# Kernel tuning notes

Hardware: AMD Instinct MI355X
Metric: run time of the kernel (lower is better)

Reference implementation:

```python
import jax, jax.numpy as jnp
import numpy as np
from jax import lax

KERNEL = 21
SHIFT = KERNEL - 1  # 20
NUM_LEVELS = 2
EPS = 1e-5
NEG_SLOPE = 0.01


def _conv1d(x, w):
    # x: [B, Cin, T], w: [Cout, Cin, K] -> [B, Cout, T-K+1]
    return lax.conv_general_dilated(x, w, window_strides=(1,), padding='VALID',
                                    dimension_numbers=('NCH', 'OIH', 'NCH'))


def _batchnorm_train(x, gamma, beta):
    # training-mode BN over (N, L) per channel, biased variance (torch semantics)
    mean = jnp.mean(x, axis=(0, 2), keepdims=True)
    var = jnp.mean((x - mean) ** 2, axis=(0, 2), keepdims=True)
    return (x - mean) * lax.rsqrt(var + EPS) * gamma[None, :, None] + beta[None, :, None]


def _spp(y, L, num_levels, pool):
    # y: [B, C, Tc]; L: [B] valid lengths. Level i has 2^i bins:
    #   bin j covers [j*floor(L/2^i), j*floor(L/2^i)+ceil(L/2^i)), matching
    #   F.max_pool1d/avg_pool1d(kernel=ceil(f), stride=floor(f)) on x[:, :, :L].
    B, C, Tc = y.shape
    pos = jnp.arange(Tc)[None, :]                     # [1, Tc]
    Lf = L.astype(jnp.float32)
    outs = []
    for i in range(num_levels):
        k = 2 ** i
        f = Lf / k
        stride = jnp.floor(f).astype(jnp.int32)        # [B]
        kern = jnp.ceil(f).astype(jnp.int32)           # [B]
        bins = []
        for j in range(k):
            start = j * stride                         # [B]
            mask = (pos >= start[:, None]) & (pos < (start + kern)[:, None])  # [B, Tc]
            m = mask[:, None, :]                       # [B, 1, Tc]
            if pool == 'max':
                bins.append(jnp.max(jnp.where(m, y, -jnp.inf), axis=-1))      # [B, C]
            else:
                s = jnp.sum(jnp.where(m, y, jnp.zeros((), y.dtype)), axis=-1)
                bins.append(s / kern[:, None].astype(y.dtype))
        # torch .view flattens (C, k) channel-major
        outs.append(jnp.stack(bins, axis=-1).reshape(B, C * k))
    return jnp.concatenate(outs, axis=1)               # [B, C*(2^n - 1)]


def setup_inputs() -> dict:
    key = jax.random.key(0)
    k1, k2, k3, k4, k5 = jax.random.split(key, 5)
    B, C, T = 32, 64, 16384
    n_tasks = 2
    n_lin = 2 * C * (2 ** NUM_LEVELS - 1)  # 384
    x = jax.random.normal(k1, (B, C, T), dtype=jnp.float32)
    orig_len = jax.random.randint(k2, (B,), T // 2, T + 1, dtype=jnp.int32)
    w1 = jax.random.normal(k3, (C, C, KERNEL), dtype=jnp.float32) * 0.05
    w2 = jax.random.normal(k4, (C, C, KERNEL), dtype=jnp.float32) * 0.05
    g1 = jnp.ones((C,), jnp.float32); b1 = jnp.zeros((C,), jnp.float32)
    g2 = jnp.ones((C,), jnp.float32); b2 = jnp.zeros((C,), jnp.float32)
    fc_w = jax.random.normal(k5, (n_tasks, n_lin), dtype=jnp.float32) * 0.05
    fc_b = jnp.zeros((n_tasks,), jnp.float32)
    return {"x": x, "orig_len": orig_len, "w1": w1, "g1": g1, "b1": b1,
            "w2": w2, "g2": g2, "b2": b2, "fc_w": fc_w, "fc_b": fc_b}


def reference(x, orig_len, w1, g1, b1, w2, g2, b2, fc_w, fc_b):
    L = orig_len - SHIFT  # valid conv-output length per sample
    y1 = jax.nn.leaky_relu(_batchnorm_train(_conv1d(x, w1), g1, b1), NEG_SLOPE)
    p1 = _spp(y1, L, NUM_LEVELS, 'max')
    y2 = jax.nn.leaky_relu(_batchnorm_train(_conv1d(x, w2), g2, b2), NEG_SLOPE)
    p2 = _spp(y2, L, NUM_LEVELS, 'avg')
    feat = jnp.concatenate([p1, p2], axis=1)           # [B, 384]
    return feat @ fc_w.T + fc_b
```

## Files before the change

kernel.cpp:

```cpp
#include <hip/hip_runtime.h>

#define AS1 __attribute__((address_space(1)))
#define AS3 __attribute__((address_space(3)))

using u16 = unsigned short;
using u32 = unsigned int;
typedef __attribute__((ext_vector_type(8))) short bf16x8;
typedef __attribute__((ext_vector_type(4))) float f32x4;

constexpr int Bn    = 32;
constexpr int Tn    = 16384;
constexpr int TCn   = 16364;
constexpr int TILE  = 256;
constexpr int XROWS = 280;
constexpr int TPAD  = 16416;

__device__ __forceinline__ u16 f2bf(float f) {
  union { float f; u32 u; } v; v.f = f;
  u32 u = v.u;
  u += 0x7fffu + ((u >> 16) & 1u);
  return (u16)(u >> 16);
}
__device__ __forceinline__ float bf2f(u32 h) {
  union { u32 u; float f; } v; v.u = h << 16; return v.f;
}
__device__ __forceinline__ u32 encf(float f) {
  union { float f; u32 u; } v; v.f = f;
  return (v.u & 0x80000000u) ? ~v.u : (v.u | 0x80000000u);
}
__device__ __forceinline__ float decf(u32 u) {
  union { u32 u; float f; } v;
  v.u = (u & 0x80000000u) ? (u ^ 0x80000000u) : ~u;
  return v.f;
}
__device__ __forceinline__ void gload_lds16(const void* g, void* l) {
  __builtin_amdgcn_global_load_lds((const AS1 u32*)g, (AS3 u32*)l, 16, 0, 0);
}
__device__ __forceinline__ float leaky(float z) { return z > 0.f ? z : 0.01f * z; }

__global__ __launch_bounds__(256) void transpose_x(const float* __restrict__ x,
                                                   u16* __restrict__ x_t,
                                                   const float* __restrict__ w1,
                                                   const float* __restrict__ w2,
                                                   u16* __restrict__ wf1,
                                                   u16* __restrict__ wf2) {
  __shared__ u16 lt[64][64];
  const int bx  = blockIdx.x;
  const int tid = threadIdx.x;

  if (bx >= Bn * 256) {
    const int bxx = bx - Bn * 256;
    const int cv  = bxx / 42;
    const int c   = bxx % 42;
    const float* w = cv ? w2 : w1;
    u16* wf = cv ? wf2 : wf1;
    const int ct   = tid >> 6;
    const int lane = tid & 63;
    const int q  = lane >> 4;
    const int rr = lane & 15;
    const int k  = c >> 1;
    const int cb = (c & 1) * 32;
    const int co = ct * 16 + rr;
    u16 us[8] __attribute__((aligned(16)));
#pragma unroll
    for (int j = 0; j < 8; ++j) {
      int ci = cb + q * 8 + j;
      us[j] = f2bf(w[((size_t)co * 64 + ci) * 21 + k]);
    }
    *(uint4*)&wf[((size_t)(c * 4 + ct) * 64 + lane) * 8] = *(const uint4*)us;
    return;
  }

  const int b   = bx >> 8;
  const int tt  = bx & 255;
  const int t0  = tt * 64;
  const int ci0 = (tid & 15) * 4;
  const int tl0 = (tid >> 4) * 4;
  float4 v[4];
#pragma unroll
  for (int j = 0; j < 4; ++j)
    v[j] = *(const float4*)(x + (size_t)(b * 64 + ci0 + j) * Tn + t0 + tl0);
  float vr[4][4] = {{v[0].x,v[0].y,v[0].z,v[0].w},{v[1].x,v[1].y,v[1].z,v[1].w},
                    {v[2].x,v[2].y,v[2].z,v[2].w},{v[3].x,v[3].y,v[3].z,v[3].w}};
#pragma unroll
  for (int e = 0; e < 4; ++e) {
    int tl = tl0 + e;
    u32 lo = (u32)f2bf(vr[0][e]) | ((u32)f2bf(vr[1][e]) << 16);
    u32 hi = (u32)f2bf(vr[2][e]) | ((u32)f2bf(vr[3][e]) << 16);
    uint2 pk = make_uint2(lo, hi);
    *(uint2*)&lt[tl][ci0] = pk;
  }
  __syncthreads();
  const int row = tid >> 2;
  const int seg = tid & 3;
  const int c0  = seg * 16;
  const int sw  = (row & 7) * 8;
  u16* op = x_t + ((size_t)b * TPAD + t0 + row) * 64 + c0;
  *(uint4*)op       = *(const uint4*)&lt[row][c0 ^ sw];
  *(uint4*)(op + 8) = *(const uint4*)&lt[row][(c0 + 8) ^ sw];
  if (tt == 0) {
    uint4 z = make_uint4(0u, 0u, 0u, 0u);
    uint4* pz = (uint4*)(x_t + ((size_t)b * TPAD + Tn) * 64);
    pz[tid] = z;
  }
}

__global__ __launch_bounds__(256, 2) void conv_mfma(const u16* __restrict__ x_t,
                                                    const u16* __restrict__ wf1,
                                                    const u16* __restrict__ wf2,
                                                    u16* __restrict__ y1,
                                                    u16* __restrict__ y2,
                                                    float* __restrict__ stats) {
  __shared__ u16 xs[XROWS * 64];
  __shared__ u16 wsw[7 * 4 * 64 * 8];
  __shared__ float sred[128];

  const int bid  = blockIdx.x;
  const int cv   = bid & 1;
  const int tmp  = bid >> 1;
  const int tile = tmp & 63;
  const int b    = tmp >> 6;
  const int t0   = tile * TILE;
  const int tid  = threadIdx.x;
  const int w    = tid >> 6;
  const int lane = tid & 63;
  const int q    = lane >> 4;
  const int r    = lane & 15;
  const u16* wf  = cv ? wf2 : wf1;

  if (tid < 128) sred[tid] = 0.f;

  const u16* xg = x_t + ((size_t)b * TPAD + t0) * 64;
  for (int s = w; s < 35; s += 4)
    gload_lds16(xg + (size_t)s * 512 + lane * 8, &xs[s * 512]);

  f32x4 acc[4][4];
#pragma unroll
  for (int a = 0; a < 4; ++a)
#pragma unroll
    for (int t = 0; t < 4; ++t)
      acc[a][t] = (f32x4){0.f, 0.f, 0.f, 0.f};

  for (int g = 0; g < 6; ++g) {
    const u16* wg = wf + (size_t)g * 14336;
    for (int s = w; s < 28; s += 4)
      gload_lds16(wg + (size_t)s * 512 + lane * 8, &wsw[s * 512]);
    __syncthreads();
#pragma unroll
    for (int cl = 0; cl < 7; ++cl) {
      const int c  = g * 7 + cl;
      const int k  = c >> 1;
      const int cb = (c & 1) * 32;
      bf16x8 af[4];
#pragma unroll
      for (int ct = 0; ct < 4; ++ct)
        af[ct] = *(const bf16x8*)&wsw[((cl * 4 + ct) * 64 + lane) * 8];
      bf16x8 bx[4];
#pragma unroll
      for (int tt = 0; tt < 4; ++tt) {
        int p = w * 64 + tt * 16 + r + k;
        int cidx = (cb + q * 8) ^ ((p & 7) * 8);
        bx[tt] = *(const bf16x8*)&xs[p * 64 + cidx];
      }
#pragma unroll
      for (int ct = 0; ct < 4; ++ct)
#pragma unroll
        for (int tt = 0; tt < 4; ++tt)
          acc[ct][tt] = __builtin_amdgcn_mfma_f32_16x16x32_bf16(af[ct], bx[tt], acc[ct][tt], 0, 0, 0);
    }
    __syncthreads();
  }

#pragma unroll
  for (int ct = 0; ct < 4; ++ct)
#pragma unroll
    for (int i = 0; i < 4; ++i) {
      float sv = 0.f, sq = 0.f;
#pragma unroll
      for (int tt = 0; tt < 4; ++tt) {
        int tg = t0 + w * 64 + tt * 16 + r;
        if (tg < TCn) {
          float v = acc[ct][tt][i];
          sv += v; sq += v * v;
        }
      }
#pragma unroll
      for (int m = 1; m < 16; m <<= 1) {
        sv += __shfl_xor(sv, m, 64);
        sq += __shfl_xor(sq, m, 64);
      }
      if (r == 0) {
        int co = ct * 16 + q * 4 + i;
        atomicAdd(&sred[co * 2], sv);
        atomicAdd(&sred[co * 2 + 1], sq);
      }
    }

  u16* ys = xs;
#pragma unroll
  for (int ct = 0; ct < 4; ++ct)
#pragma unroll
    for (int tt = 0; tt < 4; ++tt) {
      int tl = w * 64 + tt * 16 + r;
#pragma unroll
      for (int i = 0; i < 4; ++i) {
        int co = ct * 16 + q * 4 + i;
        ys[tl * 64 + co] = f2bf(acc[ct][tt][i]);
      }
    }
  __syncthreads();
  u16* yo = (cv ? y2 : y1) + ((size_t)b * Tn + t0) * 64;
#pragma unroll
  for (int m = 0; m < 8; ++m) {
    int idx = (m * 256 + tid) * 8;
    *(uint4*)(yo + idx) = *(const uint4*)(ys + idx);
  }
  if (tid < 128) atomicAdd(&stats[cv * 128 + tid], sred[tid]);
}

__global__ __launch_bounds__(256) void spp(const u16* __restrict__ y1,
                                           const u16* __restrict__ y2,
                                           const float* __restrict__ stats,
                                           const float* __restrict__ g1v,
                                           const float* __restrict__ b1v,
                                           const float* __restrict__ g2v,
                                           const float* __restrict__ b2v,
                                           const int* __restrict__ orig_len,
                                           u32* __restrict__ featU) {
  const int bx = blockIdx.x;
  const int b  = bx >> 4;
  const int ch = bx & 15;
  const int tid  = threadIdx.x;
  const int g    = tid & 15;
  const int trow = tid >> 4;
  const int co0  = g * 4;
  const int L     = orig_len[b] - 20;
  const int str2  = L >> 1;
  const int kern2 = L - str2;
  const float Nf = 32.0f * 16364.0f;
  float a1[4], c1[4], a2[4], c2[4];
#pragma unroll
  for (int j = 0; j < 4; ++j) {
    int co = co0 + j;
    float s, sq, mean, var;
    s = stats[co * 2]; sq = stats[co * 2 + 1];
    mean = s / Nf; var = sq / Nf - mean * mean; if (var < 0.f) var = 0.f;
    a1[j] = g1v[co] * rsqrtf(var + 1e-5f);
    c1[j] = b1v[co] - mean * a1[j];
    s = stats[128 + co * 2]; sq = stats[128 + co * 2 + 1];
    mean = s / Nf; var = sq / Nf - mean * mean; if (var < 0.f) var = 0.f;
    a2[j] = g2v[co] * rsqrtf(var + 1e-5f);
    c2[j] = b2v[co] - mean * a2[j];
  }
  float m1[4] = {-3.4e38f,-3.4e38f,-3.4e38f,-3.4e38f};
  float m2[4] = {-3.4e38f,-3.4e38f,-3.4e38f,-3.4e38f};
  float s0[4] = {0,0,0,0}, sb0[4] = {0,0,0,0}, sb1[4] = {0,0,0,0};
  const int tbase = ch * 1024;
  int tend = tbase + 1024;
  if (tend > L) tend = L;
  const u16* p1 = y1 + (size_t)b * Tn * 64 + co0;
  const u16* p2 = y2 + (size_t)b * Tn * 64 + co0;
  for (int t = tbase + trow; t < tend; t += 16) {
    uint2 v1 = *(const uint2*)(p1 + (size_t)t * 64);
    uint2 v2 = *(const uint2*)(p2 + (size_t)t * 64);
    float f1[4] = { bf2f(v1.x & 0xffffu), bf2f(v1.x >> 16),
                    bf2f(v1.y & 0xffffu), bf2f(v1.y >> 16) };
    float f2[4] = { bf2f(v2.x & 0xffffu), bf2f(v2.x >> 16),
                    bf2f(v2.y & 0xffffu), bf2f(v2.y >> 16) };
    bool in0 = (t < kern2), in1 = (t >= str2);
#pragma unroll
    for (int j = 0; j < 4; ++j) {
      float z1 = leaky(fmaf(a1[j], f1[j], c1[j]));
      float z2 = leaky(fmaf(a2[j], f2[j], c2[j]));
      s0[j] += z2;
      if (in0) { m1[j] = fmaxf(m1[j], z1); sb0[j] += z2; }
      if (in1) { m2[j] = fmaxf(m2[j], z1); sb1[j] += z2; }
    }
  }
#pragma unroll
  for (int m = 16; m <= 32; m <<= 1) {
#pragma unroll
    for (int j = 0; j < 4; ++j) {
      m1[j]  = fmaxf(m1[j], __shfl_xor(m1[j], m, 64));
      m2[j]  = fmaxf(m2[j], __shfl_xor(m2[j], m, 64));
      s0[j]  += __shfl_xor(s0[j],  m, 64);
      sb0[j] += __shfl_xor(sb0[j], m, 64);
      sb1[j] += __shfl_xor(sb1[j], m, 64);
    }
  }
  if (((tid & 63) >> 4) == 0) {
    u32* fb = featU + (size_t)b * 384;
    float* ff = (float*)fb;
#pragma unroll
    for (int j = 0; j < 4; ++j) {
      int co = co0 + j;
      u32 e1 = encf(m1[j]), e2 = encf(m2[j]);
      atomicMax(&fb[co], e1 > e2 ? e1 : e2);
      atomicMax(&fb[64 + co * 2], e1);
      atomicMax(&fb[64 + co * 2 + 1], e2);
      atomicAdd(&ff[192 + co], s0[j]);
      atomicAdd(&ff[256 + co * 2], sb0[j]);
      atomicAdd(&ff[256 + co * 2 + 1], sb1[j]);
    }
  }
}

__global__ void fc(const u32* __restrict__ featU,
                   const int* __restrict__ orig_len,
                   const float* __restrict__ fc_w,
                   const float* __restrict__ fc_b,
                   float* __restrict__ out) {
  const int tid  = threadIdx.x;
  const int pair = tid >> 2;
  const int part = tid & 3;
  const int b = pair >> 1;
  const int n = pair & 1;
  const int L = orig_len[b] - 20;
  const int kern2 = L - (L >> 1);
  const u32* fb = featU + (size_t)b * 384;
  const float* ff = (const float*)fb;
  float acc = 0.f;
  for (int j = part; j < 384; j += 4) {
    float fv;
    if (j < 192)      fv = decf(fb[j]);
    else if (j < 256) fv = ff[j] / (float)L;
    else              fv = ff[j] / (float)kern2;
    acc += fv * fc_w[n * 384 + j];
  }
  acc += __shfl_xor(acc, 1, 64);
  acc += __shfl_xor(acc, 2, 64);
  if (part == 0) out[b * 2 + n] = acc + fc_b[n];
}

extern "C" void kernel_launch(void* const* d_in, const int* in_sizes, int n_in,
                              void* d_out, int out_size, void* d_ws, size_t ws_size,
                              hipStream_t stream) {
  const float* x        = (const float*)d_in[0];
  const int*   orig_len = (const int*)d_in[1];
  const float* w1  = (const float*)d_in[2];
  const float* g1  = (const float*)d_in[3];
  const float* b1  = (const float*)d_in[4];
  const float* w2  = (const float*)d_in[5];
  const float* g2  = (const float*)d_in[6];
  const float* b2  = (const float*)d_in[7];
  const float* fcw = (const float*)d_in[8];
  const float* fcb = (const float*)d_in[9];
  float* out = (float*)d_out;

  char* ws = (char*)d_ws;
  const size_t XT_BYTES = (size_t)Bn * TPAD * 64 * 2;
  const size_t Y_BYTES  = (size_t)Bn * Tn * 64 * 2;
  const size_t WF_BYTES = (size_t)42 * 4 * 64 * 8 * 2;
  size_t off = 0;
  u16* x_t = (u16*)(ws + off); off += XT_BYTES;
  u16* y1  = (u16*)(ws + off); off += Y_BYTES;
  u16* y2  = (u16*)(ws + off); off += Y_BYTES;
  u16* wf1 = (u16*)(ws + off); off += WF_BYTES;
  u16* wf2 = (u16*)(ws + off); off += WF_BYTES;
  float* stats = (float*)(ws + off);
  u32*   featU = (u32*)(ws + off + 1024);
  const size_t SMALL_BYTES = 1024 + 49152;

  hipMemsetAsync(ws + off, 0, SMALL_BYTES, stream);
  transpose_x<<<Bn * 256 + 84, 256, 0, stream>>>(x, x_t, w1, w2, wf1, wf2);
  conv_mfma<<<Bn * 64 * 2, 256, 0, stream>>>(x_t, wf1, wf2, y1, y2, stats);
  spp<<<Bn * 16, 256, 0, stream>>>(y1, y2, stats, g1, b1, g2, b2, orig_len, featU);
  fc<<<1, 256, 0, stream>>>(featU, orig_len, fcw, fcb, out);
  (void)in_sizes; (void)n_in; (void)out_size; (void)ws_size;
}
```

Baseline: 483.6 us.

## Double tile size and double-buffer weight loads in conv MFMA kernel

Doubles the conv time tile to 512 so each wave computes 128 time positions, reusing each loaded weight fragment across twice as many MFMAs. It double-buffers the weight chunk in LDS, prefetching the next group during compute with raw barriers and vmcnt waits instead of two full syncthreads per group. The y staging store now writes packed 4-element bf16 with an XOR swizzle to avoid LDS bank conflicts, and the BN stats skip per-element bounds checks on full tiles. In exchange the kernel has double the accumulator registers, larger LDS use and occupancy 1, and half the blocks, which may leave CUs underused.

```diff
diff --git a/kernel.cpp b/kernel.cpp
--- a/kernel.cpp
+++ b/kernel.cpp
@@ -11,8 +11,8 @@
 constexpr int Bn    = 32;
 constexpr int Tn    = 16384;
 constexpr int TCn   = 16364;
-constexpr int TILE  = 256;
-constexpr int XROWS = 280;
+constexpr int TILE  = 512;
+constexpr int XROWS = 536;
 constexpr int TPAD  = 16416;
 
 __device__ __forceinline__ u16 f2bf(float f) {
@@ -105,21 +105,21 @@
   }
 }
 
-__global__ __launch_bounds__(256, 2) void conv_mfma(const u16* __restrict__ x_t,
+__global__ __launch_bounds__(256, 1) void conv_mfma(const u16* __restrict__ x_t,
                                                     const u16* __restrict__ wf1,
                                                     const u16* __restrict__ wf2,
                                                     u16* __restrict__ y1,
                                                     u16* __restrict__ y2,
                                                     float* __restrict__ stats) {
   __shared__ u16 xs[XROWS * 64];
-  __shared__ u16 wsw[7 * 4 * 64 * 8];
+  __shared__ u16 wsw[2][7 * 4 * 64 * 8];
   __shared__ float sred[128];
 
   const int bid  = blockIdx.x;
   const int cv   = bid & 1;
   const int tmp  = bid >> 1;
-  const int tile = tmp & 63;
-  const int b    = tmp >> 6;
+  const int tile = tmp & 31;
+  const int b    = tmp >> 5;
   const int t0   = tile * TILE;
   const int tid  = threadIdx.x;
   const int w    = tid >> 6;
@@ -131,21 +131,31 @@
   if (tid < 128) sred[tid] = 0.f;
 
   const u16* xg = x_t + ((size_t)b * TPAD + t0) * 64;
-  for (int s = w; s < 35; s += 4)
+  for (int s = w; s < 67; s += 4)
     gload_lds16(xg + (size_t)s * 512 + lane * 8, &xs[s * 512]);
-
-  f32x4 acc[4][4];
+  for (int s = w; s < 28; s += 4)
+    gload_lds16(wf + (size_t)s * 512 + lane * 8, &wsw[0][s * 512]);
+
+  f32x4 acc[4][8];
 #pragma unroll
   for (int a = 0; a < 4; ++a)
 #pragma unroll
-    for (int t = 0; t < 4; ++t)
+    for (int t = 0; t < 8; ++t)
       acc[a][t] = (f32x4){0.f, 0.f, 0.f, 0.f};
 
   for (int g = 0; g < 6; ++g) {
-    const u16* wg = wf + (size_t)g * 14336;
-    for (int s = w; s < 28; s += 4)
-      gload_lds16(wg + (size_t)s * 512 + lane * 8, &wsw[s * 512]);
-    __syncthreads();
+    __builtin_amdgcn_s_barrier();
+    if (g < 5) {
+      const u16* wg = wf + (size_t)(g + 1) * 14336;
+      for (int s = w; s < 28; s += 4)
+        gload_lds16(wg + (size_t)s * 512 + lane * 8, &wsw[(g + 1) & 1][s * 512]);
+      asm volatile("s_waitcnt vmcnt(7)" ::: "memory");
+    } else {
+      asm volatile("s_waitcnt vmcnt(0)" ::: "memory");
+    }
+    __builtin_amdgcn_s_barrier();
+    __builtin_amdgcn_sched_barrier(0);
+    const int mb = g & 1;
 #pragma unroll
     for (int cl = 0; cl < 7; ++cl) {
       const int c  = g * 7 + cl;
@@ -154,34 +164,42 @@
       bf16x8 af[4];
 #pragma unroll
       for (int ct = 0; ct < 4; ++ct)
-        af[ct] = *(const bf16x8*)&wsw[((cl * 4 + ct) * 64 + lane) * 8];
-      bf16x8 bx[4];
-#pragma unroll
-      for (int tt = 0; tt < 4; ++tt) {
-        int p = w * 64 + tt * 16 + r + k;
+        af[ct] = *(const bf16x8*)&wsw[mb][((cl * 4 + ct) * 64 + lane) * 8];
+      bf16x8 bx[8];
+#pragma unroll
+      for (int tt = 0; tt < 8; ++tt) {
+        int p = w * 128 + tt * 16 + r + k;
         int cidx = (cb + q * 8) ^ ((p & 7) * 8);
         bx[tt] = *(const bf16x8*)&xs[p * 64 + cidx];
       }
 #pragma unroll
       for (int ct = 0; ct < 4; ++ct)
 #pragma unroll
-        for (int tt = 0; tt < 4; ++tt)
+        for (int tt = 0; tt < 8; ++tt)
           acc[ct][tt] = __builtin_amdgcn_mfma_f32_16x16x32_bf16(af[ct], bx[tt], acc[ct][tt], 0, 0, 0);
     }
-    __syncthreads();
-  }
-
+  }
+
+  const bool full_t = (t0 + TILE <= TCn);
 #pragma unroll
   for (int ct = 0; ct < 4; ++ct)
 #pragma unroll
     for (int i = 0; i < 4; ++i) {
       float sv = 0.f, sq = 0.f;
-#pragma unroll
-      for (int tt = 0; tt < 4; ++tt) {
-        int tg = t0 + w * 64 + tt * 16 + r;
-        if (tg < TCn) {
+      if (full_t) {
+#pragma unroll
+        for (int tt = 0; tt < 8; ++tt) {
           float v = acc[ct][tt][i];
           sv += v; sq += v * v;
+        }
+      } else {
+#pragma unroll
+        for (int tt = 0; tt < 8; ++tt) {
+          int tg = t0 + w * 128 + tt * 16 + r;
+          if (tg < TCn) {
+            float v = acc[ct][tt][i];
+            sv += v; sq += v * v;
+          }
         }
       }
 #pragma unroll
@@ -196,24 +214,29 @@
       }
     }
 
+  __syncthreads();
+
   u16* ys = xs;
 #pragma unroll
   for (int ct = 0; ct < 4; ++ct)
 #pragma unroll
-    for (int tt = 0; tt < 4; ++tt) {
-      int tl = w * 64 + tt * 16 + r;
-#pragma unroll
-      for (int i = 0; i < 4; ++i) {
-        int co = ct * 16 + q * 4 + i;
-        ys[tl * 64 + co] = f2bf(acc[ct][tt][i]);
-      }
+    for (int tt = 0; tt < 8; ++tt) {
+      int tl = w * 128 + tt * 16 + r;
+      int sw = (tl & 7) * 8;
+      int co0 = (ct * 16 + q * 4) ^ sw;
+      u32 lo = (u32)f2bf(acc[ct][tt][0]) | ((u32)f2bf(acc[ct][tt][1]) << 16);
+      u32 hi = (u32)f2bf(acc[ct][tt][2]) | ((u32)f2bf(acc[ct][tt][3]) << 16);
+      *(uint2*)&ys[tl * 64 + co0] = make_uint2(lo, hi);
     }
   __syncthreads();
   u16* yo = (cv ? y2 : y1) + ((size_t)b * Tn + t0) * 64;
 #pragma unroll
-  for (int m = 0; m < 8; ++m) {
-    int idx = (m * 256 + tid) * 8;
-    *(uint4*)(yo + idx) = *(const uint4*)(ys + idx);
+  for (int m = 0; m < 16; ++m) {
+    int flat = m * 256 + tid;
+    int row  = flat >> 3;
+    int c0   = (flat & 7) * 8;
+    int sw   = (row & 7) * 8;
+    *(uint4*)(yo + (size_t)row * 64 + c0) = *(const uint4*)&ys[row * 64 + (c0 ^ sw)];
   }
   if (tid < 128) atomicAdd(&stats[cv * 128 + tid], sred[tid]);
 }
@@ -363,7 +386,7 @@
 
   hipMemsetAsync(ws + off, 0, SMALL_BYTES, stream);
   transpose_x<<<Bn * 256 + 84, 256, 0, stream>>>(x, x_t, w1, w2, wf1, wf2);
-  conv_mfma<<<Bn * 64 * 2, 256, 0, stream>>>(x_t, wf1, wf2, y1, y2, stats);
+  conv_mfma<<<Bn * 32 * 2, 256, 0, stream>>>(x_t, wf1, wf2, y1, y2, stats);
   spp<<<Bn * 16, 256, 0, stream>>>(y1, y2, stats, g1, b1, g2, b2, orig_len, featU);
   fc<<<1, 256, 0, stream>>>(featU, orig_len, fcw, fcb, out);
   (void)in_sizes; (void)n_in; (void)out_size; (void)ws_size;
```

New measurement: 521.5 us. 7.8% more time.

## Stream conv weights from global into registers, drop weight LDS staging and barriers

Applied to the files above, without the earlier changes.

The conv kernel no longer stages weight chunks into shared memory with per-group barriers. Each lane now loads its MFMA A-fragments straight from global memory into double-buffered registers, prefetching the next tap while the current MFMAs run, wrapped in s_setprio. Launch bounds move to 4 blocks per SM, the BN-stat masking is skipped for full tiles, and the output staging uses swizzled packed 64-bit LDS writes to cut bank conflicts. The risk is more register pressure at the higher occupancy target and global-load latency on the weight path.

```diff
diff --git a/kernel.cpp b/kernel.cpp
--- a/kernel.cpp
+++ b/kernel.cpp
@@ -105,14 +105,13 @@
   }
 }
 
-__global__ __launch_bounds__(256, 2) void conv_mfma(const u16* __restrict__ x_t,
+__global__ __launch_bounds__(256, 4) void conv_mfma(const u16* __restrict__ x_t,
                                                     const u16* __restrict__ wf1,
                                                     const u16* __restrict__ wf2,
                                                     u16* __restrict__ y1,
                                                     u16* __restrict__ y2,
                                                     float* __restrict__ stats) {
   __shared__ u16 xs[XROWS * 64];
-  __shared__ u16 wsw[7 * 4 * 64 * 8];
   __shared__ float sred[128];
 
   const int bid  = blockIdx.x;
@@ -134,6 +133,15 @@
   for (int s = w; s < 35; s += 4)
     gload_lds16(xg + (size_t)s * 512 + lane * 8, &xs[s * 512]);
 
+  const u16* wfl = wf + lane * 8;
+  bf16x8 afA[4], afB[4];
+#pragma unroll
+  for (int ct = 0; ct < 4; ++ct) afA[ct] = *(const bf16x8*)(wfl + ct * 512);
+#pragma unroll
+  for (int ct = 0; ct < 4; ++ct) afB[ct] = *(const bf16x8*)(wfl + 2048 + ct * 512);
+
+  __syncthreads();
+
   f32x4 acc[4][4];
 #pragma unroll
   for (int a = 0; a < 4; ++a)
@@ -141,47 +149,70 @@
     for (int t = 0; t < 4; ++t)
       acc[a][t] = (f32x4){0.f, 0.f, 0.f, 0.f};
 
-  for (int g = 0; g < 6; ++g) {
-    const u16* wg = wf + (size_t)g * 14336;
-    for (int s = w; s < 28; s += 4)
-      gload_lds16(wg + (size_t)s * 512 + lane * 8, &wsw[s * 512]);
-    __syncthreads();
-#pragma unroll
-    for (int cl = 0; cl < 7; ++cl) {
-      const int c  = g * 7 + cl;
-      const int k  = c >> 1;
-      const int cb = (c & 1) * 32;
-      bf16x8 af[4];
+  const int rowbase = w * 64 + r;
+
+  for (int j = 0; j < 21; ++j) {
+    const int swl  = ((rowbase + j) & 7) * 8;
+    const int cid0 = (q * 8) ^ swl;
+    const int cid1 = cid0 ^ 32;
+    {
+      bf16x8 bx[4];
+#pragma unroll
+      for (int tt = 0; tt < 4; ++tt)
+        bx[tt] = *(const bf16x8*)&xs[(rowbase + tt * 16 + j) * 64 + cid0];
+      __builtin_amdgcn_s_setprio(1);
 #pragma unroll
       for (int ct = 0; ct < 4; ++ct)
-        af[ct] = *(const bf16x8*)&wsw[((cl * 4 + ct) * 64 + lane) * 8];
+#pragma unroll
+        for (int tt = 0; tt < 4; ++tt)
+          acc[ct][tt] = __builtin_amdgcn_mfma_f32_16x16x32_bf16(afA[ct], bx[tt], acc[ct][tt], 0, 0, 0);
+      __builtin_amdgcn_s_setprio(0);
+      if (j < 20) {
+        const u16* p = wfl + (size_t)(2 * j + 2) * 2048;
+#pragma unroll
+        for (int ct = 0; ct < 4; ++ct) afA[ct] = *(const bf16x8*)(p + ct * 512);
+      }
+    }
+    {
       bf16x8 bx[4];
 #pragma unroll
-      for (int tt = 0; tt < 4; ++tt) {
-        int p = w * 64 + tt * 16 + r + k;
-        int cidx = (cb + q * 8) ^ ((p & 7) * 8);
-        bx[tt] = *(const bf16x8*)&xs[p * 64 + cidx];
+      for (int tt = 0; tt < 4; ++tt)
+        bx[tt] = *(const bf16x8*)&xs[(rowbase + tt * 16 + j) * 64 + cid1];
+      __builtin_amdgcn_s_setprio(1);
+#pragma unroll
+      for (int ct = 0; ct < 4; ++ct)
+#pragma unroll
+        for (int tt = 0; tt < 4; ++tt)
+          acc[ct][tt] = __builtin_amdgcn_mfma_f32_16x16x32_bf16(afB[ct], bx[tt], acc[ct][tt], 0, 0, 0);
+      __builtin_amdgcn_s_setprio(0);
+      if (j < 20) {
+        const u16* p = wfl + (size_t)(2 * j + 3) * 2048;
+#pragma unroll
+        for (int ct = 0; ct < 4; ++ct) afB[ct] = *(const bf16x8*)(p + ct * 512);
       }
-#pragma unroll
-      for (int ct = 0; ct < 4; ++ct)
-#pragma unroll
-        for (int tt = 0; tt < 4; ++tt)
-          acc[ct][tt] = __builtin_amdgcn_mfma_f32_16x16x32_bf16(af[ct], bx[tt], acc[ct][tt], 0, 0, 0);
-    }
-    __syncthreads();
-  }
-
+    }
+  }
+
+  const bool full_t = (t0 + TILE <= TCn);
 #pragma unroll
   for (int ct = 0; ct < 4; ++ct)
 #pragma unroll
     for (int i = 0; i < 4; ++i) {
       float sv = 0.f, sq = 0.f;
-#pragma unroll
-      for (int tt = 0; tt < 4; ++tt) {
-        int tg = t0 + w * 64 + tt * 16 + r;
-        if (tg < TCn) {
+      if (full_t) {
+#pragma unroll
+        for (int tt = 0; tt < 4; ++tt) {
           float v = acc[ct][tt][i];
           sv += v; sq += v * v;
+        }
+      } else {
+#pragma unroll
+        for (int tt = 0; tt < 4; ++tt) {
+          int tg = t0 + w * 64 + tt * 16 + r;
+          if (tg < TCn) {
+            float v = acc[ct][tt][i];
+            sv += v; sq += v * v;
+          }
         }
       }
 #pragma unroll
@@ -196,24 +227,29 @@
       }
     }
 
+  __syncthreads();
+
   u16* ys = xs;
 #pragma unroll
   for (int ct = 0; ct < 4; ++ct)
 #pragma unroll
     for (int tt = 0; tt < 4; ++tt) {
       int tl = w * 64 + tt * 16 + r;
-#pragma unroll
-      for (int i = 0; i < 4; ++i) {
-        int co = ct * 16 + q * 4 + i;
-        ys[tl * 64 + co] = f2bf(acc[ct][tt][i]);
-      }
+      int sw = (tl & 7) * 8;
+      int co0 = (ct * 16 + q * 4) ^ sw;
+      u32 lo = (u32)f2bf(acc[ct][tt][0]) | ((u32)f2bf(acc[ct][tt][1]) << 16);
+      u32 hi = (u32)f2bf(acc[ct][tt][2]) | ((u32)f2bf(acc[ct][tt][3]) << 16);
+      *(uint2*)&ys[tl * 64 + co0] = make_uint2(lo, hi);
     }
   __syncthreads();
   u16* yo = (cv ? y2 : y1) + ((size_t)b * Tn + t0) * 64;
 #pragma unroll
   for (int m = 0; m < 8; ++m) {
-    int idx = (m * 256 + tid) * 8;
-    *(uint4*)(yo + idx) = *(const uint4*)(ys + idx);
+    int flat = m * 256 + tid;
+    int row  = flat >> 3;
+    int c0   = (flat & 7) * 8;
+    int sw   = (row & 7) * 8;
+    *(uint4*)(yo + (size_t)row * 64 + c0) = *(const uint4*)&ys[row * 64 + (c0 ^ sw)];
   }
   if (tid < 128) atomicAdd(&stats[cv * 128 + tid], sred[tid]);
 }
```

Result: faster. 466.1 us (-3.6%).
